# Optimization experiments

Measured on AMD Instinct MI355X. Metric: run time of the kernel, lower is better.

## Reference

```python
import jax, jax.numpy as jnp
import numpy as np

N_NODES = 100000
N_GAMES = 1600000


def gcn_conv(x, W, b, edge_index, num_nodes):
    """PyG GCNConv: out = D^-1/2 (A + I) D^-1/2 (x W) + b."""
    src, dst = edge_index[0], edge_index[1]
    xw = x @ W  # [N, out]
    # degree with self-loops
    deg = jax.ops.segment_sum(jnp.ones(src.shape[0], x.dtype), dst,
                              num_segments=num_nodes) + 1.0
    dinv = jax.lax.rsqrt(deg)  # deg >= 1 so safe
    norm = dinv[src] * dinv[dst]  # [E]
    msg = jax.ops.segment_sum(xw[src] * norm[:, None], dst,
                              num_segments=num_nodes)
    # self-loop contribution: norm_ii = dinv[i]^2
    return msg + xw * (dinv * dinv)[:, None] + b


def setup_inputs() -> dict:
    key = jax.random.key(0)
    ks = jax.random.split(key, 12)
    x = jax.random.normal(ks[0], (N_NODES, 7), dtype=jnp.float32)
    w2b = jax.random.randint(ks[1], (2, N_GAMES), 0, N_NODES, dtype=jnp.int64)
    # edge_index = cat(w2b, b2w) as in the source
    edge_index = jnp.concatenate([w2b, w2b[::-1]], axis=1)
    h1, h2, h3, h4 = 8, 16, 32, 4

    def lin(k, fan_in, fan_out):
        kw, kb = jax.random.split(k)
        bound = 1.0 / np.sqrt(fan_in)
        W = jax.random.uniform(kw, (fan_in, fan_out), jnp.float32, -bound, bound)
        b = jax.random.uniform(kb, (fan_out,), jnp.float32, -bound, bound)
        return W, b

    W1, b1 = lin(ks[2], 7, h1)
    W2, b2 = lin(ks[3], h1, h2)
    W3, b3 = lin(ks[4], h2, h3)
    lw1, lb1 = lin(ks[5], 2 * h3, h4)
    lw2, lb2 = lin(ks[6], h4, 3)
    return {"x": x, "edge_index": edge_index, "w2b": w2b,
            "W1": W1, "b1": b1, "W2": W2, "b2": b2, "W3": W3, "b3": b3,
            "lw1": lw1, "lb1": lb1, "lw2": lw2, "lb2": lb2}


def reference(x, edge_index, w2b, W1, b1, W2, b2, W3, b3, lw1, lb1, lw2, lb2):
    h = jax.nn.relu(gcn_conv(x, W1, b1, edge_index, N_NODES))
    h = jax.nn.relu(gcn_conv(h, W2, b2, edge_index, N_NODES))
    h = jax.nn.relu(gcn_conv(h, W3, b3, edge_index, N_NODES))
    # vectorized replacement of the per-edge Python loop: gather + concat
    concat = jnp.concatenate([h[w2b[0]], h[w2b[1]]], axis=1)  # [E, 2*h3]
    hidden = concat @ lw1 + lb1
    edge_pred = hidden @ lw2 + lb2  # [E, 3]
    return edge_pred
```

## Files before the change

kernel.cpp:

```cpp
#include <hip/hip_runtime.h>

static constexpr int N_NODES = 100000;
static constexpr int N_GAMES = 1600000;
static constexpr int SHIFT   = 7;
static constexpr int BSIZE   = 1 << SHIFT;
static constexpr int NB1     = (N_NODES + BSIZE - 1) / BSIZE;
static constexpr int CAP     = 4608;
static constexpr int TILE_E  = 4096;

__global__ void coarse_scatter_kernel(const int* __restrict__ wa, const int* __restrict__ wb,
                                      int* __restrict__ gcur, unsigned* __restrict__ packed,
                                      int n) {
    __shared__ int lh[NB1];
    __shared__ int lbase[NB1];
    for (int t = threadIdx.x; t < NB1; t += blockDim.x) lh[t] = 0;
    __syncthreads();
    int e0 = blockIdx.x * TILE_E;
    int e1 = e0 + TILE_E; if (e1 > n) e1 = n;
    for (int e = e0 + threadIdx.x; e < e1; e += blockDim.x) {
        int a = wa[e], b = wb[e];
        atomicAdd(&lh[b >> SHIFT], 1);
        atomicAdd(&lh[a >> SHIFT], 1);
    }
    __syncthreads();
    for (int t = threadIdx.x; t < NB1; t += blockDim.x) {
        int c = lh[t];
        if (c) lbase[t] = atomicAdd(&gcur[t], c);
        lh[t] = 0;
    }
    __syncthreads();
    for (int e = e0 + threadIdx.x; e < e1; e += blockDim.x) {
        int a = wa[e], b = wb[e];
        int bk1 = b >> SHIFT;
        int r1 = lbase[bk1] + atomicAdd(&lh[bk1], 1);
        if (r1 < CAP) packed[(size_t)bk1 * CAP + r1] = ((unsigned)a << SHIFT) | (unsigned)(b & (BSIZE - 1));
        int bk2 = a >> SHIFT;
        int r2 = lbase[bk2] + atomicAdd(&lh[bk2], 1);
        if (r2 < CAP) packed[(size_t)bk2 * CAP + r2] = ((unsigned)b << SHIFT) | (unsigned)(a & (BSIZE - 1));
    }
}

__global__ void fine_sort_kernel(const int* __restrict__ gcur, const unsigned* __restrict__ packed,
                                 int* __restrict__ off, int* __restrict__ deg, int* __restrict__ adj) {
    __shared__ int lh[BSIZE];
    __shared__ int buf[BSIZE];
    __shared__ int foff[BSIZE];
    int bkt = blockIdx.x;
    int size = gcur[bkt]; if (size > CAP) size = CAP;
    int base = bkt * CAP;
    int t = threadIdx.x;
    if (t < BSIZE) lh[t] = 0;
    __syncthreads();
    for (int k = t; k < size; k += blockDim.x)
        atomicAdd(&lh[packed[base + k] & (BSIZE - 1)], 1);
    __syncthreads();
    if (t < BSIZE) buf[t] = lh[t];
    __syncthreads();
    for (int d = 1; d < BSIZE; d <<= 1) {
        int add = (t < BSIZE && t >= d) ? buf[t - d] : 0;
        __syncthreads();
        if (t < BSIZE) buf[t] += add;
        __syncthreads();
    }
    if (t < BSIZE) {
        int excl = buf[t] - lh[t];
        foff[t] = excl;
        int node = bkt * BSIZE + t;
        if (node < N_NODES) {
            off[node] = base + excl;
            deg[node] = lh[t];
        }
        lh[t] = 0;
    }
    __syncthreads();
    for (int k = t; k < size; k += blockDim.x) {
        unsigned u = packed[base + k];
        int d = (int)(u & (BSIZE - 1));
        int r = atomicAdd(&lh[d], 1);
        adj[base + foff[d] + r] = (int)(u >> SHIFT);
    }
}

__global__ void dinv_from_deg_kernel(const int* __restrict__ deg, float* __restrict__ dinv, int n) {
    int i = blockIdx.x * blockDim.x + threadIdx.x;
    if (i < n) dinv[i] = rsqrtf((float)deg[i] + 1.0f);
}

template<int FIN, int FOUT>
__global__ void node_linear_scaled_kernel(const float* __restrict__ h, const float* __restrict__ W,
                                          const float* __restrict__ dinv,
                                          float* __restrict__ xws, int n) {
    __shared__ float sW[FIN * FOUT];
    for (int k = threadIdx.x; k < FIN * FOUT; k += blockDim.x) sW[k] = W[k];
    __syncthreads();
    int i = blockIdx.x * blockDim.x + threadIdx.x;
    if (i >= n) return;
    float hin[FIN];
#pragma unroll
    for (int k = 0; k < FIN; ++k) hin[k] = h[(size_t)i * FIN + k];
    float d = dinv[i];
#pragma unroll
    for (int j = 0; j < FOUT; ++j) {
        float acc = 0.0f;
#pragma unroll
        for (int k = 0; k < FIN; ++k) acc += hin[k] * sW[k * FOUT + j];
        xws[(size_t)i * FOUT + j] = acc * d;
    }
}

template<int FOUT>
__global__ void gather_combine_kernel(const int* __restrict__ off, const int* __restrict__ deg,
                                      const int* __restrict__ adj,
                                      const float* __restrict__ dinv, const float* __restrict__ xws,
                                      const float* __restrict__ bias, float* __restrict__ out, int n) {
    constexpr int Q = FOUT / 4;
    int i = blockIdx.x * blockDim.x + threadIdx.x;
    if (i >= n) return;
    const float4* x4 = reinterpret_cast<const float4*>(xws);
    float4 acc[Q];
    size_t self = (size_t)i * Q;
#pragma unroll
    for (int j = 0; j < Q; ++j) acc[j] = x4[self + j];
    int lo = off[i], hi = lo + deg[i];
    for (int k = lo; k < hi; ++k) {
        int nb = adj[k];
        size_t rb = (size_t)nb * Q;
#pragma unroll
        for (int j = 0; j < Q; ++j) {
            float4 v = x4[rb + j];
            acc[j].x += v.x; acc[j].y += v.y; acc[j].z += v.z; acc[j].w += v.w;
        }
    }
    float d = dinv[i];
#pragma unroll
    for (int j = 0; j < Q; ++j) {
        float4 r;
        r.x = fmaxf(acc[j].x * d + bias[j * 4 + 0], 0.0f);
        r.y = fmaxf(acc[j].y * d + bias[j * 4 + 1], 0.0f);
        r.z = fmaxf(acc[j].z * d + bias[j * 4 + 2], 0.0f);
        r.w = fmaxf(acc[j].w * d + bias[j * 4 + 3], 0.0f);
        reinterpret_cast<float4*>(out)[self + j] = r;
    }
}

__global__ void gather_project32_kernel(const int* __restrict__ off, const int* __restrict__ deg,
                                        const int* __restrict__ adj,
                                        const float* __restrict__ dinv, const float* __restrict__ xws,
                                        const float* __restrict__ b3, const float* __restrict__ lw1,
                                        float4* __restrict__ pa4, float4* __restrict__ pb4, int n) {
    __shared__ float sW[256];
    __shared__ float sB[32];
    for (int k = threadIdx.x; k < 256; k += blockDim.x) sW[k] = lw1[k];
    if (threadIdx.x < 32) sB[threadIdx.x] = b3[threadIdx.x];
    __syncthreads();
    int i = blockIdx.x * blockDim.x + threadIdx.x;
    if (i >= n) return;
    const float4* x4 = reinterpret_cast<const float4*>(xws);
    float4 acc[8];
    size_t self = (size_t)i * 8;
#pragma unroll
    for (int j = 0; j < 8; ++j) acc[j] = x4[self + j];
    int lo = off[i], hi = lo + deg[i];
    for (int k = lo; k < hi; ++k) {
        int nb = adj[k];
        size_t rb = (size_t)nb * 8;
#pragma unroll
        for (int j = 0; j < 8; ++j) {
            float4 v = x4[rb + j];
            acc[j].x += v.x; acc[j].y += v.y; acc[j].z += v.z; acc[j].w += v.w;
        }
    }
    float d = dinv[i];
    float h3[32];
#pragma unroll
    for (int j = 0; j < 8; ++j) {
        h3[j * 4 + 0] = fmaxf(acc[j].x * d + sB[j * 4 + 0], 0.0f);
        h3[j * 4 + 1] = fmaxf(acc[j].y * d + sB[j * 4 + 1], 0.0f);
        h3[j * 4 + 2] = fmaxf(acc[j].z * d + sB[j * 4 + 2], 0.0f);
        h3[j * 4 + 3] = fmaxf(acc[j].w * d + sB[j * 4 + 3], 0.0f);
    }
    float pa[4] = {0.f, 0.f, 0.f, 0.f};
    float pb[4] = {0.f, 0.f, 0.f, 0.f};
#pragma unroll
    for (int k = 0; k < 32; ++k) {
#pragma unroll
        for (int j = 0; j < 4; ++j) {
            pa[j] += h3[k] * sW[k * 4 + j];
            pb[j] += h3[k] * sW[(32 + k) * 4 + j];
        }
    }
    pa4[i] = make_float4(pa[0], pa[1], pa[2], pa[3]);
    pb4[i] = make_float4(pb[0], pb[1], pb[2], pb[3]);
}

__global__ void edge_mlp_pab_kernel(const int* __restrict__ wa, const int* __restrict__ wb,
                                    const float4* __restrict__ pa4, const float4* __restrict__ pb4,
                                    const float* __restrict__ lb1, const float* __restrict__ lw2,
                                    const float* __restrict__ lb2,
                                    float* __restrict__ out, int ngames) {
    __shared__ float sB1[4];
    __shared__ float sW2[12];
    __shared__ float sB2[3];
    if (threadIdx.x < 4) sB1[threadIdx.x] = lb1[threadIdx.x];
    if (threadIdx.x < 12) sW2[threadIdx.x] = lw2[threadIdx.x];
    if (threadIdx.x < 3) sB2[threadIdx.x] = lb2[threadIdx.x];
    __syncthreads();
    int e = blockIdx.x * blockDim.x + threadIdx.x;
    if (e >= ngames) return;
    int a = wa[e], b = wb[e];
    float4 A = pa4[a];
    float4 B = pb4[b];
    float h0 = A.x + B.x + sB1[0];
    float h1 = A.y + B.y + sB1[1];
    float h2 = A.z + B.z + sB1[2];
    float h3 = A.w + B.w + sB1[3];
    float p0 = sB2[0] + h0 * sW2[0] + h1 * sW2[3] + h2 * sW2[6] + h3 * sW2[9];
    float p1 = sB2[1] + h0 * sW2[1] + h1 * sW2[4] + h2 * sW2[7] + h3 * sW2[10];
    float p2 = sB2[2] + h0 * sW2[2] + h1 * sW2[5] + h2 * sW2[8] + h3 * sW2[11];
    out[(size_t)e * 3 + 0] = p0;
    out[(size_t)e * 3 + 1] = p1;
    out[(size_t)e * 3 + 2] = p2;
}

extern "C" void kernel_launch(void* const* d_in, const int* in_sizes, int n_in,
                              void* d_out, int out_size, void* d_ws, size_t ws_size,
                              hipStream_t stream) {
    (void)in_sizes; (void)n_in; (void)out_size; (void)ws_size;
    const float* x   = (const float*)d_in[0];
    const int*   w2b = (const int*)d_in[2];
    const float* W1  = (const float*)d_in[3];
    const float* b1  = (const float*)d_in[4];
    const float* W2  = (const float*)d_in[5];
    const float* b2  = (const float*)d_in[6];
    const float* W3  = (const float*)d_in[7];
    const float* b3  = (const float*)d_in[8];
    const float* lw1 = (const float*)d_in[9];
    const float* lb1 = (const float*)d_in[10];
    const float* lw2 = (const float*)d_in[11];
    const float* lb2 = (const float*)d_in[12];
    float* out = (float*)d_out;

    char* ws = (char*)d_ws;
    size_t o = 0;
    auto alloc = [&](size_t bytes) -> void* {
        void* p = ws + o;
        o = (o + bytes + 255) & ~(size_t)255;
        return p;
    };
    int*      gcur   = (int*)     alloc((size_t)NB1 * 4);
    int*      off    = (int*)     alloc((size_t)N_NODES * 4);
    int*      deg    = (int*)     alloc((size_t)N_NODES * 4);
    float*    dinv   = (float*)   alloc((size_t)N_NODES * 4);
    unsigned* packed = (unsigned*)alloc((size_t)NB1 * CAP * 4);
    int*      adj    = (int*)     alloc((size_t)NB1 * CAP * 4);

    constexpr size_t PA_OFF = (size_t)8  << 20;
    constexpr size_t PB_OFF = (size_t)10 << 20;
    float*  hbuf = (float*)packed;
    float4* pa4  = (float4*)((char*)packed + PA_OFF);
    float4* pb4  = (float4*)((char*)packed + PB_OFF);
    float* xws = out;

    const int* wa = w2b;
    const int* wb = w2b + N_GAMES;

    const int BLK = 256;
    auto grid = [](long n, int blk) { return dim3((unsigned)((n + blk - 1) / blk)); };

    (void)hipMemsetAsync(gcur, 0, (size_t)NB1 * 4, stream);
    coarse_scatter_kernel<<<grid(N_GAMES, TILE_E), BLK, 0, stream>>>(wa, wb, gcur, packed, N_GAMES);
    fine_sort_kernel<<<NB1, BLK, 0, stream>>>(gcur, packed, off, deg, adj);
    dinv_from_deg_kernel<<<grid(N_NODES, BLK), BLK, 0, stream>>>(deg, dinv, N_NODES);

    node_linear_scaled_kernel<7, 8><<<grid(N_NODES, BLK), BLK, 0, stream>>>(x, W1, dinv, xws, N_NODES);
    gather_combine_kernel<8><<<grid(N_NODES, BLK), BLK, 0, stream>>>(off, deg, adj, dinv, xws, b1, hbuf, N_NODES);

    node_linear_scaled_kernel<8, 16><<<grid(N_NODES, BLK), BLK, 0, stream>>>(hbuf, W2, dinv, xws, N_NODES);
    gather_combine_kernel<16><<<grid(N_NODES, BLK), BLK, 0, stream>>>(off, deg, adj, dinv, xws, b2, hbuf, N_NODES);

    node_linear_scaled_kernel<16, 32><<<grid(N_NODES, BLK), BLK, 0, stream>>>(hbuf, W3, dinv, xws, N_NODES);
    gather_project32_kernel<<<grid(N_NODES, BLK), BLK, 0, stream>>>(off, deg, adj, dinv, xws, b3, lw1, pa4, pb4, N_NODES);

    edge_mlp_pab_kernel<<<grid(N_GAMES, BLK), BLK, 0, stream>>>(wa, wb, pa4, pb4, lb1, lw2, lb2, out, N_GAMES);
}
```

Measured before the change: 428.3 us.

## Aggregate before linear transform and split node gathers across four lanes

Reorders each GCN layer to aggregate the narrower input features (pre-scaled by dinv) first and then apply the weight matrix, fusing the separate node_linear kernels into the gather kernels. Each node is now handled by four threads that each gather a slice of the feature row, then exchange slices with shuffles before the matmul. This cuts gathered bytes per edge (8/8/16 floats instead of 8/16/32) and removes three launches and intermediate writes. The cost is more shuffles, four times as many threads each walking the same adjacency list, and new workspace buffer offsets that must not overlap.

```diff
diff --git a/kernel.cpp b/kernel.cpp
--- a/kernel.cpp
+++ b/kernel.cpp
@@ -86,111 +86,145 @@
     if (i < n) dinv[i] = rsqrtf((float)deg[i] + 1.0f);
 }
 
-template<int FIN, int FOUT>
-__global__ void node_linear_scaled_kernel(const float* __restrict__ h, const float* __restrict__ W,
-                                          const float* __restrict__ dinv,
-                                          float* __restrict__ xws, int n) {
-    __shared__ float sW[FIN * FOUT];
-    for (int k = threadIdx.x; k < FIN * FOUT; k += blockDim.x) sW[k] = W[k];
-    __syncthreads();
-    int i = blockIdx.x * blockDim.x + threadIdx.x;
-    if (i >= n) return;
-    float hin[FIN];
-#pragma unroll
-    for (int k = 0; k < FIN; ++k) hin[k] = h[(size_t)i * FIN + k];
-    float d = dinv[i];
-#pragma unroll
-    for (int j = 0; j < FOUT; ++j) {
-        float acc = 0.0f;
-#pragma unroll
-        for (int k = 0; k < FIN; ++k) acc += hin[k] * sW[k * FOUT + j];
-        xws[(size_t)i * FOUT + j] = acc * d;
-    }
-}
-
-template<int FOUT>
-__global__ void gather_combine_kernel(const int* __restrict__ off, const int* __restrict__ deg,
+__global__ void scale_pad_x_kernel(const float* __restrict__ x, const float* __restrict__ dinv,
+                                   float* __restrict__ hs0, int n) {
+    int tid = blockIdx.x * blockDim.x + threadIdx.x;
+    if (tid >= n * 8) return;
+    int i = tid >> 3, f = tid & 7;
+    hs0[tid] = (f < 7) ? x[i * 7 + f] * dinv[i] : 0.0f;
+}
+
+template<int KUSE, int FOUT>
+__global__ void gather_linear8_kernel(const int* __restrict__ off, const int* __restrict__ deg,
                                       const int* __restrict__ adj,
-                                      const float* __restrict__ dinv, const float* __restrict__ xws,
-                                      const float* __restrict__ bias, float* __restrict__ out, int n) {
-    constexpr int Q = FOUT / 4;
-    int i = blockIdx.x * blockDim.x + threadIdx.x;
-    if (i >= n) return;
-    const float4* x4 = reinterpret_cast<const float4*>(xws);
-    float4 acc[Q];
-    size_t self = (size_t)i * Q;
-#pragma unroll
-    for (int j = 0; j < Q; ++j) acc[j] = x4[self + j];
+                                      const float* __restrict__ dinv, const float* __restrict__ src,
+                                      const float* __restrict__ W, const float* __restrict__ bias,
+                                      float* __restrict__ dst, int n) {
+    __shared__ float sW[KUSE * FOUT];
+    __shared__ float sB[FOUT];
+    for (int k = threadIdx.x; k < KUSE * FOUT; k += blockDim.x) sW[k] = W[k];
+    if (threadIdx.x < FOUT) sB[threadIdx.x] = bias[threadIdx.x];
+    __syncthreads();
+    int tid = blockIdx.x * blockDim.x + threadIdx.x;
+    if (tid >= n * 4) return;
+    int i = tid >> 2;
+    int h = tid & 3;
+    const float2* x2 = reinterpret_cast<const float2*>(src);
+    float2 acc = x2[(size_t)i * 4 + h];
     int lo = off[i], hi = lo + deg[i];
     for (int k = lo; k < hi; ++k) {
         int nb = adj[k];
-        size_t rb = (size_t)nb * Q;
-#pragma unroll
-        for (int j = 0; j < Q; ++j) {
-            float4 v = x4[rb + j];
-            acc[j].x += v.x; acc[j].y += v.y; acc[j].z += v.z; acc[j].w += v.w;
-        }
-    }
+        float2 v = x2[(size_t)nb * 4 + h];
+        acc.x += v.x; acc.y += v.y;
+    }
+    float p0 = __shfl_xor(acc.x, 1);
+    float p1 = __shfl_xor(acc.y, 1);
+    bool o1 = (h & 1);
+    float q0 = o1 ? p0 : acc.x;
+    float q1 = o1 ? p1 : acc.y;
+    float q2 = o1 ? acc.x : p0;
+    float q3 = o1 ? acc.y : p1;
+    float r0 = __shfl_xor(q0, 2);
+    float r1 = __shfl_xor(q1, 2);
+    float r2 = __shfl_xor(q2, 2);
+    float r3 = __shfl_xor(q3, 2);
+    bool o2 = (h & 2);
+    float s[8];
+    s[0] = o2 ? r0 : q0;  s[1] = o2 ? r1 : q1;
+    s[2] = o2 ? r2 : q2;  s[3] = o2 ? r3 : q3;
+    s[4] = o2 ? q0 : r0;  s[5] = o2 ? q1 : r1;
+    s[6] = o2 ? q2 : r2;  s[7] = o2 ? q3 : r3;
     float d = dinv[i];
-#pragma unroll
-    for (int j = 0; j < Q; ++j) {
-        float4 r;
-        r.x = fmaxf(acc[j].x * d + bias[j * 4 + 0], 0.0f);
-        r.y = fmaxf(acc[j].y * d + bias[j * 4 + 1], 0.0f);
-        r.z = fmaxf(acc[j].z * d + bias[j * 4 + 2], 0.0f);
-        r.w = fmaxf(acc[j].w * d + bias[j * 4 + 3], 0.0f);
-        reinterpret_cast<float4*>(out)[self + j] = r;
-    }
-}
-
-__global__ void gather_project32_kernel(const int* __restrict__ off, const int* __restrict__ deg,
+    constexpr int FO = FOUT / 4;
+    int j0 = h * FO;
+    float r[FO];
+#pragma unroll
+    for (int jj = 0; jj < FO; ++jj) {
+        float t = 0.0f;
+#pragma unroll
+        for (int k = 0; k < KUSE; ++k) t += s[k] * sW[k * FOUT + j0 + jj];
+        r[jj] = fmaxf(d * t + sB[j0 + jj], 0.0f) * d;
+    }
+    if constexpr (FO == 2) {
+        reinterpret_cast<float2*>(dst)[(size_t)i * 4 + h] = make_float2(r[0], r[1]);
+    } else {
+        float4 w4; w4.x = r[0]; w4.y = r[1]; w4.z = r[2]; w4.w = r[3];
+        reinterpret_cast<float4*>(dst)[(size_t)i * 4 + h] = w4;
+    }
+}
+
+__global__ void gather_project16_kernel(const int* __restrict__ off, const int* __restrict__ deg,
                                         const int* __restrict__ adj,
-                                        const float* __restrict__ dinv, const float* __restrict__ xws,
-                                        const float* __restrict__ b3, const float* __restrict__ lw1,
+                                        const float* __restrict__ dinv, const float* __restrict__ src,
+                                        const float* __restrict__ W3, const float* __restrict__ b3,
+                                        const float* __restrict__ lw1,
                                         float4* __restrict__ pa4, float4* __restrict__ pb4, int n) {
-    __shared__ float sW[256];
+    __shared__ float sW[512];
+    __shared__ float sLW[256];
     __shared__ float sB[32];
-    for (int k = threadIdx.x; k < 256; k += blockDim.x) sW[k] = lw1[k];
+    for (int k = threadIdx.x; k < 512; k += blockDim.x) sW[k] = W3[k];
+    if (threadIdx.x < 256) sLW[threadIdx.x] = lw1[threadIdx.x];
     if (threadIdx.x < 32) sB[threadIdx.x] = b3[threadIdx.x];
     __syncthreads();
-    int i = blockIdx.x * blockDim.x + threadIdx.x;
-    if (i >= n) return;
-    const float4* x4 = reinterpret_cast<const float4*>(xws);
-    float4 acc[8];
-    size_t self = (size_t)i * 8;
-#pragma unroll
-    for (int j = 0; j < 8; ++j) acc[j] = x4[self + j];
+    int tid = blockIdx.x * blockDim.x + threadIdx.x;
+    if (tid >= n * 4) return;
+    int i = tid >> 2;
+    int h = tid & 3;
+    const float4* x4 = reinterpret_cast<const float4*>(src);
+    float4 acc = x4[(size_t)i * 4 + h];
     int lo = off[i], hi = lo + deg[i];
     for (int k = lo; k < hi; ++k) {
         int nb = adj[k];
-        size_t rb = (size_t)nb * 8;
-#pragma unroll
-        for (int j = 0; j < 8; ++j) {
-            float4 v = x4[rb + j];
-            acc[j].x += v.x; acc[j].y += v.y; acc[j].z += v.z; acc[j].w += v.w;
-        }
+        float4 v = x4[(size_t)nb * 4 + h];
+        acc.x += v.x; acc.y += v.y; acc.z += v.z; acc.w += v.w;
+    }
+    float a0 = acc.x, a1 = acc.y, a2 = acc.z, a3 = acc.w;
+    float p0 = __shfl_xor(a0, 1), p1 = __shfl_xor(a1, 1),
+          p2 = __shfl_xor(a2, 1), p3 = __shfl_xor(a3, 1);
+    bool o1 = (h & 1);
+    float q[8];
+    q[0] = o1 ? p0 : a0;  q[1] = o1 ? p1 : a1;
+    q[2] = o1 ? p2 : a2;  q[3] = o1 ? p3 : a3;
+    q[4] = o1 ? a0 : p0;  q[5] = o1 ? a1 : p1;
+    q[6] = o1 ? a2 : p2;  q[7] = o1 ? a3 : p3;
+    float rr[8];
+#pragma unroll
+    for (int k = 0; k < 8; ++k) rr[k] = __shfl_xor(q[k], 2);
+    bool o2 = (h & 2);
+    float s[16];
+#pragma unroll
+    for (int k = 0; k < 8; ++k) {
+        s[k]     = o2 ? rr[k] : q[k];
+        s[8 + k] = o2 ? q[k]  : rr[k];
     }
     float d = dinv[i];
-    float h3[32];
-#pragma unroll
-    for (int j = 0; j < 8; ++j) {
-        h3[j * 4 + 0] = fmaxf(acc[j].x * d + sB[j * 4 + 0], 0.0f);
-        h3[j * 4 + 1] = fmaxf(acc[j].y * d + sB[j * 4 + 1], 0.0f);
-        h3[j * 4 + 2] = fmaxf(acc[j].z * d + sB[j * 4 + 2], 0.0f);
-        h3[j * 4 + 3] = fmaxf(acc[j].w * d + sB[j * 4 + 3], 0.0f);
-    }
+    int j0 = h * 8;
     float pa[4] = {0.f, 0.f, 0.f, 0.f};
     float pb[4] = {0.f, 0.f, 0.f, 0.f};
 #pragma unroll
-    for (int k = 0; k < 32; ++k) {
-#pragma unroll
-        for (int j = 0; j < 4; ++j) {
-            pa[j] += h3[k] * sW[k * 4 + j];
-            pb[j] += h3[k] * sW[(32 + k) * 4 + j];
+    for (int jj = 0; jj < 8; ++jj) {
+        int j = j0 + jj;
+        float t = 0.0f;
+#pragma unroll
+        for (int k = 0; k < 16; ++k) t += s[k] * sW[k * 32 + j];
+        float h3v = fmaxf(d * t + sB[j], 0.0f);
+#pragma unroll
+        for (int c = 0; c < 4; ++c) {
+            pa[c] += h3v * sLW[j * 4 + c];
+            pb[c] += h3v * sLW[(32 + j) * 4 + c];
         }
     }
-    pa4[i] = make_float4(pa[0], pa[1], pa[2], pa[3]);
-    pb4[i] = make_float4(pb[0], pb[1], pb[2], pb[3]);
+#pragma unroll
+    for (int c = 0; c < 4; ++c) {
+        pa[c] += __shfl_xor(pa[c], 1);
+        pa[c] += __shfl_xor(pa[c], 2);
+        pb[c] += __shfl_xor(pb[c], 1);
+        pb[c] += __shfl_xor(pb[c], 2);
+    }
+    if (h == 0) {
+        pa4[i] = make_float4(pa[0], pa[1], pa[2], pa[3]);
+        pb4[i] = make_float4(pb[0], pb[1], pb[2], pb[3]);
+    }
 }
 
 __global__ void edge_mlp_pab_kernel(const int* __restrict__ wa, const int* __restrict__ wb,
@@ -254,12 +288,11 @@
     unsigned* packed = (unsigned*)alloc((size_t)NB1 * CAP * 4);
     int*      adj    = (int*)     alloc((size_t)NB1 * CAP * 4);
 
-    constexpr size_t PA_OFF = (size_t)8  << 20;
-    constexpr size_t PB_OFF = (size_t)10 << 20;
-    float*  hbuf = (float*)packed;
-    float4* pa4  = (float4*)((char*)packed + PA_OFF);
-    float4* pb4  = (float4*)((char*)packed + PB_OFF);
-    float* xws = out;
+    float*  hs0 = (float*)packed;
+    float4* pa4 = (float4*)packed;
+    float4* pb4 = (float4*)((char*)packed + 0x1A0000);
+    float*  h1s = (float*)((char*)packed + 0x340000);
+    float*  h2s = (float*)((char*)packed + 0x680000);
 
     const int* wa = w2b;
     const int* wb = w2b + N_GAMES;
@@ -272,14 +305,16 @@
     fine_sort_kernel<<<NB1, BLK, 0, stream>>>(gcur, packed, off, deg, adj);
     dinv_from_deg_kernel<<<grid(N_NODES, BLK), BLK, 0, stream>>>(deg, dinv, N_NODES);
 
-    node_linear_scaled_kernel<7, 8><<<grid(N_NODES, BLK), BLK, 0, stream>>>(x, W1, dinv, xws, N_NODES);
-    gather_combine_kernel<8><<<grid(N_NODES, BLK), BLK, 0, stream>>>(off, deg, adj, dinv, xws, b1, hbuf, N_NODES);
-
-    node_linear_scaled_kernel<8, 16><<<grid(N_NODES, BLK), BLK, 0, stream>>>(hbuf, W2, dinv, xws, N_NODES);
-    gather_combine_kernel<16><<<grid(N_NODES, BLK), BLK, 0, stream>>>(off, deg, adj, dinv, xws, b2, hbuf, N_NODES);
-
-    node_linear_scaled_kernel<16, 32><<<grid(N_NODES, BLK), BLK, 0, stream>>>(hbuf, W3, dinv, xws, N_NODES);
-    gather_project32_kernel<<<grid(N_NODES, BLK), BLK, 0, stream>>>(off, deg, adj, dinv, xws, b3, lw1, pa4, pb4, N_NODES);
+    scale_pad_x_kernel<<<grid(8L * N_NODES, BLK), BLK, 0, stream>>>(x, dinv, hs0, N_NODES);
+
+    gather_linear8_kernel<7, 8><<<grid(4L * N_NODES, BLK), BLK, 0, stream>>>(
+        off, deg, adj, dinv, hs0, W1, b1, h1s, N_NODES);
+
+    gather_linear8_kernel<8, 16><<<grid(4L * N_NODES, BLK), BLK, 0, stream>>>(
+        off, deg, adj, dinv, h1s, W2, b2, h2s, N_NODES);
+
+    gather_project16_kernel<<<grid(4L * N_NODES, BLK), BLK, 0, stream>>>(
+        off, deg, adj, dinv, h2s, W3, b3, lw1, pa4, pb4, N_NODES);
 
     edge_mlp_pab_kernel<<<grid(N_GAMES, BLK), BLK, 0, stream>>>(wa, wb, pa4, pb4, lb1, lw2, lb2, out, N_GAMES);
 }
```

Result: faster. 347.5 us (-18.9%).
